# Optimization experiments

Measured on AMD Instinct MI355X. Metric: run time of the kernel, lower is better.

## Reference

```python
import jax, jax.numpy as jnp
import numpy as np

B, N, E = 64, 256, 2048          # graphs per batch, nodes per subgraph, edges per subgraph
V, D, H = 50000, 128, 4          # vocab_size, hidden_dim, heads
NEG_SLOPE = 0.2                  # PyG GATConv default LeakyReLU slope


def setup_inputs() -> dict:
    key = jax.random.key(0)
    ks = jax.random.split(key, 16)
    s = 0.05
    return {
        "neighbors_node1": jax.random.randint(ks[0], (B, N), 0, V),
        "neighbors_node2": jax.random.randint(ks[1], (B, N), 0, V),
        "adj1": jax.random.randint(ks[2], (B, 2, E), 0, N),
        "adj2": jax.random.randint(ks[3], (B, 2, E), 0, N),
        "emb": jax.random.normal(ks[4], (V + 1, D), jnp.float32) * 0.02,
        # GATConv 1: lin weight [H*D, D], att_src/att_dst [H, D], bias [D] (concat=False)
        "W1": jax.random.normal(ks[5], (H * D, D), jnp.float32) * s,
        "att_src1": jax.random.normal(ks[6], (H, D), jnp.float32) * s,
        "att_dst1": jax.random.normal(ks[7], (H, D), jnp.float32) * s,
        "b1": jnp.zeros((D,), jnp.float32),
        # GATConv 2
        "W2": jax.random.normal(ks[8], (H * D, D), jnp.float32) * s,
        "att_src2": jax.random.normal(ks[9], (H, D), jnp.float32) * s,
        "att_dst2": jax.random.normal(ks[10], (H, D), jnp.float32) * s,
        "b2": jnp.zeros((D,), jnp.float32),
        # final MLP: Linear(2D -> 1)
        "mlp_w": jax.random.normal(ks[11], (1, 2 * D), jnp.float32) * s,
        "mlp_b": jnp.zeros((1,), jnp.float32),
    }


def _gat_conv(x, edge_index, W, a_src, a_dst, bias):
    """PyG GATConv, concat=False (mean over heads), with self-loops.
    x: [N, D] node features; edge_index: [2, E] (row=src j, col=dst i)."""
    xh = (x @ W.T).reshape(N, H, D)                      # [N, H, D]
    loop = jnp.arange(N)
    src = jnp.concatenate([edge_index[0], loop])          # [E+N]
    dst = jnp.concatenate([edge_index[1], loop])
    asrc = jnp.einsum('nhd,hd->nh', xh, a_src)            # [N, H]
    adst = jnp.einsum('nhd,hd->nh', xh, a_dst)
    e = jax.nn.leaky_relu(asrc[src] + adst[dst], NEG_SLOPE)   # [E+N, H]
    # softmax over incoming edges of each dst node
    m = jax.ops.segment_max(e, dst, num_segments=N)
    ex = jnp.exp(e - m[dst])
    denom = jax.ops.segment_sum(ex, dst, num_segments=N)
    alpha = ex / denom[dst]                               # [E+N, H]
    out = jax.ops.segment_sum(xh[src] * alpha[:, :, None], dst, num_segments=N)  # [N, H, D]
    return out.mean(axis=1) + bias                        # [N, D]


def reference(neighbors_node1, neighbors_node2, adj1, adj2, emb,
              W1, att_src1, att_dst1, b1,
              W2, att_src2, att_dst2, b2,
              mlp_w, mlp_b):
    f1 = jax.vmap(lambda n, ei: _gat_conv(emb[n], ei, W1, att_src1, att_dst1, b1))(
        neighbors_node1, adj1)                            # [B, N, D]
    f2 = jax.vmap(lambda n, ei: _gat_conv(emb[n], ei, W2, att_src2, att_dst2, b2))(
        neighbors_node2, adj2)
    feats = jnp.concatenate([f1[:, 0], f2[:, 0]], axis=-1)  # center node of each subgraph -> [B, 2D]
    return (feats @ mlp_w.T + mlp_b)[:, 0]                # [B]
```

## Files before the change

### kernel.cpp

```cpp
#include <hip/hip_runtime.h>
#include <hip/hip_bf16.h>

#define Bg 64
#define Nn 256
#define Ee 2048
#define Dd 128
#define Hh 4
#define MAXJ 40
#define RS 132

__device__ __forceinline__ float bf2f(unsigned short u) {
    return __uint_as_float(((unsigned)u) << 16);
}

__global__ __launch_bounds__(256) void precompute_kernel(
    const void* W1, const void* as1, const void* ad1, const void* b1,
    const void* W2, const void* as2, const void* ad2, const void* b2,
    const void* mlpw, const void* mlpb, float* wv)
{
    __shared__ float s_av[3 * Dd];
    __shared__ float s_part[8 * 3 * Dd];
    __shared__ float s_red[2];
    __shared__ int   s_f32;

    const int tid = threadIdx.x;
    const int x = blockIdx.x;
    const int l = x >> 2, h = x & 3;

    if (tid < 64) {
        float v = bf2f(((const unsigned short*)W1)[tid]);
        bool bad = !(v > -64.f && v < 64.f);
        unsigned long long m = __ballot(bad);
        if (tid == 0) s_f32 = (m != 0ull) ? 1 : 0;
    }
    __syncthreads();
    const int f32 = s_f32;

    for (int i = tid; i < 3 * Dd; i += 256) {
        int t = i >> 7, d = i & 127;
        const void* p; long off;
        if (t == 0)      { p = l ? as2 : as1; off = (long)h * Dd + d; }
        else if (t == 1) { p = l ? ad2 : ad1; off = (long)h * Dd + d; }
        else             { p = mlpw;          off = (long)l * Dd + d; }
        s_av[i] = f32 ? ((const float*)p)[off]
                      : bf2f(((const unsigned short*)p)[off]);
    }
    __syncthreads();

    {
        const int kc = (tid & 31) * 4;
        const int d0 = (tid >> 5) * 16;
        float acc[3][4] = {};
        if (f32) {
            const float* Wf = (const float*)(l ? W2 : W1) + (long)h * Dd * Dd;
            #pragma unroll
            for (int dd = 0; dd < 16; ++dd) {
                int d = d0 + dd;
                float4 w = *(const float4*)(Wf + (long)d * Dd + kc);
                #pragma unroll
                for (int t = 0; t < 3; ++t) {
                    float a = s_av[t * Dd + d];
                    acc[t][0] += a * w.x; acc[t][1] += a * w.y;
                    acc[t][2] += a * w.z; acc[t][3] += a * w.w;
                }
            }
        } else {
            const unsigned short* Wb =
                (const unsigned short*)(l ? W2 : W1) + (long)h * Dd * Dd;
            #pragma unroll
            for (int dd = 0; dd < 16; ++dd) {
                int d = d0 + dd;
                ushort4 u = *(const ushort4*)(Wb + (long)d * Dd + kc);
                float wx = bf2f(u.x), wy = bf2f(u.y);
                float wz = bf2f(u.z), ww = bf2f(u.w);
                #pragma unroll
                for (int t = 0; t < 3; ++t) {
                    float a = s_av[t * Dd + d];
                    acc[t][0] += a * wx; acc[t][1] += a * wy;
                    acc[t][2] += a * wz; acc[t][3] += a * ww;
                }
            }
        }
        const int dg = tid >> 5;
        #pragma unroll
        for (int t = 0; t < 3; ++t)
            *(float4*)&s_part[(dg * 3 + t) * Dd + kc] =
                make_float4(acc[t][0], acc[t][1], acc[t][2], acc[t][3]);
    }
    __syncthreads();

    for (int i = tid; i < 3 * Dd; i += 256) {
        int t = i >> 7, k = i & 127;
        float s = 0.f;
        #pragma unroll
        for (int g = 0; g < 8; ++g) s += s_part[(g * 3 + t) * Dd + k];
        wv[((l * 3 + t) * 4 + h) * Dd + k] = s;
    }

    if (h == 0) {
        float p = 0.f;
        if (tid < 128) {
            const void* bias = l ? b2 : b1;
            float bv = f32 ? ((const float*)bias)[tid]
                           : bf2f(((const unsigned short*)bias)[tid]);
            p = bv * s_av[2 * Dd + tid];
        }
        #pragma unroll
        for (int off = 32; off > 0; off >>= 1) p += __shfl_down(p, off);
        if (tid == 0 || tid == 64) s_red[tid >> 6] = p;
        __syncthreads();
        if (tid == 0) {
            float a = s_red[0] + s_red[1];
            if (l == 0) a += f32 ? ((const float*)mlpb)[0]
                                 : bf2f(((const unsigned short*)mlpb)[0]);
            wv[3072 + l] = a;
        }
    }
}

__global__ __launch_bounds__(512) void gat_main_kernel(
    const int* nn1, const int* nn2, const int* adj1, const int* adj2,
    const void* emb, const void* W1, const float* wv, void* out)
{
    __shared__ float s_wv[24 * RS];
    __shared__ float s_rows[2 * MAXJ * RS];
    __shared__ int   s_nodes[2][Nn];
    __shared__ int   s_srcj[2][MAXJ];
    __shared__ int   s_gid[2 * MAXJ];
    __shared__ int   s_cnt[2];
    __shared__ int   s_f32;
    __shared__ float s_ps[2 * MAXJ * Hh], s_pm[2 * MAXJ * Hh];
    __shared__ float s_pd[2 * Hh], s_hval[2 * Hh], s_bdot[2];

    const int tid = threadIdx.x;
    const int b = blockIdx.x;

    const int* adjp0 = adj1 + (long)b * 2 * Ee;
    const int* adjp1 = adj2 + (long)b * 2 * Ee;
    int4 d0 = ((const int4*)(adjp0 + Ee))[tid];
    int4 s0 = ((const int4*)adjp0)[tid];
    int4 d1 = ((const int4*)(adjp1 + Ee))[tid];
    int4 s1 = ((const int4*)adjp1)[tid];

    {
        int l = tid >> 8, n = tid & 255;
        s_nodes[l][n] = (l ? nn2 : nn1)[b * Nn + n];
    }
    if (tid < 2) s_cnt[tid] = 0;

    if (tid < 64) {
        float v = bf2f(((const unsigned short*)W1)[tid]);
        bool bad = !(v > -64.f && v < 64.f);
        unsigned long long m = __ballot(bad);
        if (tid == 0) s_f32 = (m != 0ull) ? 1 : 0;
    }
    __syncthreads();
    const int f32 = s_f32;

    {
        #define SCAN1(c, sv, l) \
            if ((c) == 0) { int p = atomicAdd(&s_cnt[l], 1); \
                            if (p < MAXJ - 1) s_srcj[l][p] = (sv); }
        SCAN1(d0.x, s0.x, 0) SCAN1(d0.y, s0.y, 0)
        SCAN1(d0.z, s0.z, 0) SCAN1(d0.w, s0.w, 0)
        SCAN1(d1.x, s1.x, 1) SCAN1(d1.y, s1.y, 1)
        SCAN1(d1.z, s1.z, 1) SCAN1(d1.w, s1.w, 1)
        #undef SCAN1
    }

    for (int i = tid; i < 768; i += 512) {
        float4 f = ((const float4*)wv)[i];
        int el = i * 4, row = el >> 7, k = el & 127;
        *(float4*)&s_wv[row * RS + k] = f;
    }
    if (tid < 2) s_bdot[tid] = wv[3072 + tid];
    __syncthreads();

    int c0 = s_cnt[0]; if (c0 > MAXJ - 1) c0 = MAXJ - 1; c0 += 1;
    int c1 = s_cnt[1]; if (c1 > MAXJ - 1) c1 = MAXJ - 1; c1 += 1;
    const int tot = c0 + c1;

    if (tid < 2 * MAXJ) {
        int l = tid >= MAXJ;
        int j = l ? tid - MAXJ : tid;
        int cl = l ? c1 : c0;
        int base = l ? c0 : 0;
        if (j < cl) {
            int src = (j == cl - 1) ? 0 : s_srcj[l][j];
            s_gid[base + j] = s_nodes[l][src];
        }
    }
    __syncthreads();

    if (f32) {
        for (int idx = tid; idx < tot * 32; idx += 512) {
            int j = idx >> 5, k4 = (idx & 31) << 2;
            long gid = s_gid[j];
            float4 f = ((const float4*)emb)[gid * 32 + (k4 >> 2)];
            *(float4*)&s_rows[j * RS + k4] = f;
        }
    } else {
        for (int idx = tid; idx < tot * 16; idx += 512) {
            int j = idx >> 4, k8 = (idx & 15) << 3;
            long gid = s_gid[j];
            uint4 u = *(const uint4*)((const unsigned short*)emb + gid * Dd + k8);
            float4 f0 = make_float4(bf2f(u.x & 0xffff), bf2f(u.x >> 16),
                                    bf2f(u.y & 0xffff), bf2f(u.y >> 16));
            float4 f1 = make_float4(bf2f(u.z & 0xffff), bf2f(u.z >> 16),
                                    bf2f(u.w & 0xffff), bf2f(u.w >> 16));
            *(float4*)&s_rows[j * RS + k8] = f0;
            *(float4*)&s_rows[j * RS + k8 + 4] = f1;
        }
    }
    __syncthreads();

    const int ntask = tot * 8 + 8;
    for (int task = tid; task < ntask; task += 512) {
        int j, h, t, l;
        if (task < tot * 8) {
            j = task >> 3; h = (task >> 1) & 3; t = (task & 1) ? 2 : 0;
            l = (j < c0) ? 0 : 1;
        } else {
            int z = task - tot * 8;
            l = z >> 2; h = z & 3; t = 1;
            j = l ? (tot - 1) : (c0 - 1);
        }
        const float* wrow = s_wv + ((l * 3 + t) * Hh + h) * RS;
        const float* row  = s_rows + j * RS;
        float acc = 0.f;
        #pragma unroll 8
        for (int k = 0; k < Dd; ++k) acc += row[k] * wrow[k];
        if (task < tot * 8) {
            if (task & 1) s_pm[j * Hh + h] = acc;
            else          s_ps[j * Hh + h] = acc;
        } else {
            s_pd[(l << 2) | h] = acc;
        }
    }
    __syncthreads();

    {
        const int w = tid >> 6, lane = tid & 63;
        const int l = w >> 2, h = w & 3;
        const int j0 = l ? c0 : 0;
        const int cntl = (l ? tot : c0) - j0;
        const float pd = s_pd[w];
        const bool valid = lane < cntl;
        const int j = j0 + (valid ? lane : 0);
        float e = valid ? (s_ps[j * Hh + h] + pd) : -1e30f;
        e = (e >= 0.f) ? e : 0.2f * e;
        float m = e;
        #pragma unroll
        for (int off = 32; off > 0; off >>= 1)
            m = fmaxf(m, __shfl_xor(m, off));
        float ex = valid ? expf(e - m) : 0.f;
        float pm = valid ? s_pm[j * Hh + h] : 0.f;
        float den = ex, num = ex * pm;
        #pragma unroll
        for (int off = 32; off > 0; off >>= 1) {
            den += __shfl_xor(den, off);
            num += __shfl_xor(num, off);
        }
        if (lane == 0) s_hval[w] = num / den;
    }
    __syncthreads();

    if (tid == 0) {
        float r = 0.25f * (s_hval[0] + s_hval[1] + s_hval[2] + s_hval[3]) + s_bdot[0]
                + 0.25f * (s_hval[4] + s_hval[5] + s_hval[6] + s_hval[7]) + s_bdot[1];
        if (f32) ((float*)out)[b] = r;
        else     ((__hip_bfloat16*)out)[b] = __float2bfloat16(r);
    }
}

extern "C" void kernel_launch(void* const* d_in, const int* in_sizes, int n_in,
                              void* d_out, int out_size, void* d_ws, size_t ws_size,
                              hipStream_t stream) {
    const int* nn1  = (const int*)d_in[0];
    const int* nn2  = (const int*)d_in[1];
    const int* adj1 = (const int*)d_in[2];
    const int* adj2 = (const int*)d_in[3];
    float* wv = (float*)d_ws;

    precompute_kernel<<<8, 256, 0, stream>>>(
        d_in[5],   d_in[6],   d_in[7],
        d_in[8],
        d_in[9],   d_in[10],  d_in[11],
        d_in[12],
        d_in[13],  d_in[14],  wv);

    gat_main_kernel<<<Bg, 512, 0, stream>>>(
        nn1, nn2, adj1, adj2, d_in[4] , d_in[5] , wv, d_out);
}
```

Before: 104.3 us.

## Fuse weight precompute into main GAT kernel with flag-based inter-block sync

```diff
diff --git a/kernel.cpp b/kernel.cpp
--- a/kernel.cpp
+++ b/kernel.cpp
@@ -8,119 +8,19 @@
 #define Hh 4
 #define MAXJ 40
 #define RS 132
+#define MAGIC 0x9E3779B1u
 
 __device__ __forceinline__ float bf2f(unsigned short u) {
     return __uint_as_float(((unsigned)u) << 16);
 }
 
-__global__ __launch_bounds__(256) void precompute_kernel(
+__global__ __launch_bounds__(512) void gat_fused_kernel(
+    const int* nn1, const int* nn2, const int* adj1, const int* adj2,
+    const void* emb,
     const void* W1, const void* as1, const void* ad1, const void* b1,
     const void* W2, const void* as2, const void* ad2, const void* b2,
-    const void* mlpw, const void* mlpb, float* wv)
-{
-    __shared__ float s_av[3 * Dd];
-    __shared__ float s_part[8 * 3 * Dd];
-    __shared__ float s_red[2];
-    __shared__ int   s_f32;
-
-    const int tid = threadIdx.x;
-    const int x = blockIdx.x;
-    const int l = x >> 2, h = x & 3;
-
-    if (tid < 64) {
-        float v = bf2f(((const unsigned short*)W1)[tid]);
-        bool bad = !(v > -64.f && v < 64.f);
-        unsigned long long m = __ballot(bad);
-        if (tid == 0) s_f32 = (m != 0ull) ? 1 : 0;
-    }
-    __syncthreads();
-    const int f32 = s_f32;
-
-    for (int i = tid; i < 3 * Dd; i += 256) {
-        int t = i >> 7, d = i & 127;
-        const void* p; long off;
-        if (t == 0)      { p = l ? as2 : as1; off = (long)h * Dd + d; }
-        else if (t == 1) { p = l ? ad2 : ad1; off = (long)h * Dd + d; }
-        else             { p = mlpw;          off = (long)l * Dd + d; }
-        s_av[i] = f32 ? ((const float*)p)[off]
-                      : bf2f(((const unsigned short*)p)[off]);
-    }
-    __syncthreads();
-
-    {
-        const int kc = (tid & 31) * 4;
-        const int d0 = (tid >> 5) * 16;
-        float acc[3][4] = {};
-        if (f32) {
-            const float* Wf = (const float*)(l ? W2 : W1) + (long)h * Dd * Dd;
-            #pragma unroll
-            for (int dd = 0; dd < 16; ++dd) {
-                int d = d0 + dd;
-                float4 w = *(const float4*)(Wf + (long)d * Dd + kc);
-                #pragma unroll
-                for (int t = 0; t < 3; ++t) {
-                    float a = s_av[t * Dd + d];
-                    acc[t][0] += a * w.x; acc[t][1] += a * w.y;
-                    acc[t][2] += a * w.z; acc[t][3] += a * w.w;
-                }
-            }
-        } else {
-            const unsigned short* Wb =
-                (const unsigned short*)(l ? W2 : W1) + (long)h * Dd * Dd;
-            #pragma unroll
-            for (int dd = 0; dd < 16; ++dd) {
-                int d = d0 + dd;
-                ushort4 u = *(const ushort4*)(Wb + (long)d * Dd + kc);
-                float wx = bf2f(u.x), wy = bf2f(u.y);
-                float wz = bf2f(u.z), ww = bf2f(u.w);
-                #pragma unroll
-                for (int t = 0; t < 3; ++t) {
-                    float a = s_av[t * Dd + d];
-                    acc[t][0] += a * wx; acc[t][1] += a * wy;
-                    acc[t][2] += a * wz; acc[t][3] += a * ww;
-                }
-            }
-        }
-        const int dg = tid >> 5;
-        #pragma unroll
-        for (int t = 0; t < 3; ++t)
-            *(float4*)&s_part[(dg * 3 + t) * Dd + kc] =
-                make_float4(acc[t][0], acc[t][1], acc[t][2], acc[t][3]);
-    }
-    __syncthreads();
-
-    for (int i = tid; i < 3 * Dd; i += 256) {
-        int t = i >> 7, k = i & 127;
-        float s = 0.f;
-        #pragma unroll
-        for (int g = 0; g < 8; ++g) s += s_part[(g * 3 + t) * Dd + k];
-        wv[((l * 3 + t) * 4 + h) * Dd + k] = s;
-    }
-
-    if (h == 0) {
-        float p = 0.f;
-        if (tid < 128) {
-            const void* bias = l ? b2 : b1;
-            float bv = f32 ? ((const float*)bias)[tid]
-                           : bf2f(((const unsigned short*)bias)[tid]);
-            p = bv * s_av[2 * Dd + tid];
-        }
-        #pragma unroll
-        for (int off = 32; off > 0; off >>= 1) p += __shfl_down(p, off);
-        if (tid == 0 || tid == 64) s_red[tid >> 6] = p;
-        __syncthreads();
-        if (tid == 0) {
-            float a = s_red[0] + s_red[1];
-            if (l == 0) a += f32 ? ((const float*)mlpb)[0]
-                                 : bf2f(((const unsigned short*)mlpb)[0]);
-            wv[3072 + l] = a;
-        }
-    }
-}
-
-__global__ __launch_bounds__(512) void gat_main_kernel(
-    const int* nn1, const int* nn2, const int* adj1, const int* adj2,
-    const void* emb, const void* W1, const float* wv, void* out)
+    const void* mlpw, const void* mlpb,
+    float* wv, int f32arg, void* out)
 {
     __shared__ float s_wv[24 * RS];
     __shared__ float s_rows[2 * MAXJ * RS];
@@ -131,9 +31,117 @@
     __shared__ int   s_f32;
     __shared__ float s_ps[2 * MAXJ * Hh], s_pm[2 * MAXJ * Hh];
     __shared__ float s_pd[2 * Hh], s_hval[2 * Hh], s_bdot[2];
+    __shared__ float s_red[2];
 
     const int tid = threadIdx.x;
-    const int b = blockIdx.x;
+    const int x = blockIdx.x;
+
+    if (x < 8) {
+        const int l = x >> 2, h = x & 3;
+        float* s_av   = s_wv;
+        float* s_part = s_rows;
+
+        int f32 = f32arg;
+        if (f32 < 0) {
+            if (tid < 64) {
+                float v = bf2f(((const unsigned short*)W1)[tid]);
+                unsigned long long m = __ballot(!(v > -64.f && v < 64.f));
+                if (tid == 0) s_f32 = (m != 0ull) ? 1 : 0;
+            }
+            __syncthreads();
+            f32 = s_f32;
+        }
+
+        if (tid < 384) {
+            int t = tid >> 7, d = tid & 127;
+            const void* p; long off;
+            if (t == 0)      { p = l ? as2 : as1; off = (long)h * Dd + d; }
+            else if (t == 1) { p = l ? ad2 : ad1; off = (long)h * Dd + d; }
+            else             { p = mlpw;          off = (long)l * Dd + d; }
+            s_av[tid] = f32 ? ((const float*)p)[off]
+                            : bf2f(((const unsigned short*)p)[off]);
+        }
+        __syncthreads();
+
+        {
+            const int kc = (tid & 31) * 4;
+            const int dg = tid >> 5;
+            const int d0 = dg * 8;
+            float acc[3][4] = {};
+            if (f32) {
+                const float* Wf = (const float*)(l ? W2 : W1) + (long)h * Dd * Dd;
+                #pragma unroll
+                for (int dd = 0; dd < 8; ++dd) {
+                    int d = d0 + dd;
+                    float4 w = *(const float4*)(Wf + (long)d * Dd + kc);
+                    #pragma unroll
+                    for (int t = 0; t < 3; ++t) {
+                        float a = s_av[t * Dd + d];
+                        acc[t][0] += a * w.x; acc[t][1] += a * w.y;
+                        acc[t][2] += a * w.z; acc[t][3] += a * w.w;
+                    }
+                }
+            } else {
+                const unsigned short* Wb =
+                    (const unsigned short*)(l ? W2 : W1) + (long)h * Dd * Dd;
+                #pragma unroll
+                for (int dd = 0; dd < 8; ++dd) {
+                    int d = d0 + dd;
+                    ushort4 u = *(const ushort4*)(Wb + (long)d * Dd + kc);
+                    float wx = bf2f(u.x), wy = bf2f(u.y);
+                    float wz = bf2f(u.z), ww = bf2f(u.w);
+                    #pragma unroll
+                    for (int t = 0; t < 3; ++t) {
+                        float a = s_av[t * Dd + d];
+                        acc[t][0] += a * wx; acc[t][1] += a * wy;
+                        acc[t][2] += a * wz; acc[t][3] += a * ww;
+                    }
+                }
+            }
+            const int dg2 = tid >> 5;
+            #pragma unroll
+            for (int t = 0; t < 3; ++t)
+                *(float4*)&s_part[(dg2 * 3 + t) * Dd + kc] =
+                    make_float4(acc[t][0], acc[t][1], acc[t][2], acc[t][3]);
+        }
+        __syncthreads();
+
+        if (tid < 384) {
+            int t = tid >> 7, k = tid & 127;
+            float s = 0.f;
+            #pragma unroll
+            for (int g = 0; g < 16; ++g) s += s_part[(g * 3 + t) * Dd + k];
+            wv[((l * 3 + t) * 4 + h) * Dd + k] = s;
+        }
+
+        if (h == 0) {
+            float p = 0.f;
+            if (tid < 128) {
+                const void* bias = l ? b2 : b1;
+                float bv = f32 ? ((const float*)bias)[tid]
+                               : bf2f(((const unsigned short*)bias)[tid]);
+                p = bv * s_av[2 * Dd + tid];
+            }
+            #pragma unroll
+            for (int off = 32; off > 0; off >>= 1) p += __shfl_down(p, off);
+            if (tid == 0 || tid == 64) s_red[tid >> 6] = p;
+            __syncthreads();
+            if (tid == 0) {
+                float a = s_red[0] + s_red[1];
+                if (l == 0) a += f32 ? ((const float*)mlpb)[0]
+                                     : bf2f(((const unsigned short*)mlpb)[0]);
+                wv[3072 + l] = a;
+            }
+        }
+
+        __threadfence();
+        __syncthreads();
+        if (tid == 0)
+            atomicExch((unsigned*)wv + 3080 + x, MAGIC);
+        return;
+    }
+
+    const int b = x - 8;
 
     const int* adjp0 = adj1 + (long)b * 2 * Ee;
     const int* adjp1 = adj2 + (long)b * 2 * Ee;
@@ -148,14 +156,14 @@
     }
     if (tid < 2) s_cnt[tid] = 0;
 
-    if (tid < 64) {
+    int f32 = f32arg;
+    if (f32 < 0 && tid < 64) {
         float v = bf2f(((const unsigned short*)W1)[tid]);
-        bool bad = !(v > -64.f && v < 64.f);
-        unsigned long long m = __ballot(bad);
+        unsigned long long m = __ballot(!(v > -64.f && v < 64.f));
         if (tid == 0) s_f32 = (m != 0ull) ? 1 : 0;
     }
     __syncthreads();
-    const int f32 = s_f32;
+    if (f32 < 0) f32 = s_f32;
 
     {
         #define SCAN1(c, sv, l) \
@@ -167,13 +175,6 @@
         SCAN1(d1.z, s1.z, 1) SCAN1(d1.w, s1.w, 1)
         #undef SCAN1
     }
-
-    for (int i = tid; i < 768; i += 512) {
-        float4 f = ((const float4*)wv)[i];
-        int el = i * 4, row = el >> 7, k = el & 127;
-        *(float4*)&s_wv[row * RS + k] = f;
-    }
-    if (tid < 2) s_bdot[tid] = wv[3072 + tid];
     __syncthreads();
 
     int c0 = s_cnt[0]; if (c0 > MAXJ - 1) c0 = MAXJ - 1; c0 += 1;
@@ -212,6 +213,20 @@
             *(float4*)&s_rows[j * RS + k8 + 4] = f1;
         }
     }
+
+    if (tid < 8) {
+        unsigned* fl = (unsigned*)wv + 3080 + tid;
+        while (atomicAdd(fl, 0u) != MAGIC) __builtin_amdgcn_s_sleep(2);
+    }
+    __syncthreads();
+    __threadfence();
+
+    for (int i = tid; i < 768; i += 512) {
+        float4 f = ((const float4*)wv)[i];
+        int el = i * 4, row = el >> 7, k = el & 127;
+        *(float4*)&s_wv[row * RS + k] = f;
+    }
+    if (tid < 2) s_bdot[tid] = wv[3072 + tid];
     __syncthreads();
 
     const int ntask = tot * 8 + 8;
@@ -225,11 +240,14 @@
             l = z >> 2; h = z & 3; t = 1;
             j = l ? (tot - 1) : (c0 - 1);
         }
-        const float* wrow = s_wv + ((l * 3 + t) * Hh + h) * RS;
-        const float* row  = s_rows + j * RS;
+        const float4* r4 = (const float4*)(s_rows + j * RS);
+        const float4* w4 = (const float4*)(s_wv + ((l * 3 + t) * Hh + h) * RS);
         float acc = 0.f;
         #pragma unroll 8
-        for (int k = 0; k < Dd; ++k) acc += row[k] * wrow[k];
+        for (int k = 0; k < 32; ++k) {
+            float4 a = r4[k], w = w4[k];
+            acc += a.x * w.x + a.y * w.y + a.z * w.z + a.w * w.w;
+        }
         if (task < tot * 8) {
             if (task & 1) s_pm[j * Hh + h] = acc;
             else          s_ps[j * Hh + h] = acc;
@@ -276,19 +294,21 @@
 extern "C" void kernel_launch(void* const* d_in, const int* in_sizes, int n_in,
                               void* d_out, int out_size, void* d_ws, size_t ws_size,
                               hipStream_t stream) {
-    const int* nn1  = (const int*)d_in[0];
-    const int* nn2  = (const int*)d_in[1];
-    const int* adj1 = (const int*)d_in[2];
-    const int* adj2 = (const int*)d_in[3];
     float* wv = (float*)d_ws;
 
-    precompute_kernel<<<8, 256, 0, stream>>>(
+    int sz5 = (in_sizes && n_in > 5) ? in_sizes[5] : 0;
+    int f32arg = (sz5 == 512 * 128 * 4) ? 1 : ((sz5 == 512 * 128 * 2) ? 0 : -1);
+
+    gat_fused_kernel<<<8 + Bg, 512, 0, stream>>>(
+        (const int*)d_in[0],
+        (const int*)d_in[1],
+        (const int*)d_in[2],
+        (const int*)d_in[3],
+        d_in[4],
         d_in[5],   d_in[6],   d_in[7],
         d_in[8],
         d_in[9],   d_in[10],  d_in[11],
         d_in[12],
-        d_in[13],  d_in[14],  wv);
-
-    gat_main_kernel<<<Bg, 512, 0, stream>>>(
-        nn1, nn2, adj1, adj2, d_in[4] , d_in[5] , wv, d_out);
+        d_in[13],  d_in[14],
+        wv, f32arg, d_out);
 }
```

After: 111.5 us. +6.9%, slower.
